# Kernel tuning notes

Measured on AMD Instinct MI355X. Metric: run time of the kernel, lower is better.

Reference implementation:

```python
import jax, jax.numpy as jnp
import numpy as np

N_NODES = 100000
FEAT = 64
HID = 128
N_EDGES = 1200000


def setup_inputs() -> dict:
    key = jax.random.key(0)
    ks = jax.random.split(key, 8)
    x = jax.random.normal(ks[0], (N_NODES, FEAT), dtype=jnp.float32)
    edge_index = jax.random.randint(ks[1], (2, N_EDGES), 0, N_NODES, dtype=jnp.int32)
    # SAGEConv params: lin_l (on aggregated neighbors, with bias), lin_r (on root, no bias)
    W1l = jax.random.normal(ks[2], (HID, FEAT), jnp.float32) / np.float32(np.sqrt(FEAT))
    b1l = jnp.zeros((HID,), jnp.float32)
    W1r = jax.random.normal(ks[3], (HID, FEAT), jnp.float32) / np.float32(np.sqrt(FEAT))
    W2l = jax.random.normal(ks[4], (FEAT, HID), jnp.float32) / np.float32(np.sqrt(HID))
    b2l = jnp.zeros((FEAT,), jnp.float32)
    W2r = jax.random.normal(ks[5], (FEAT, HID), jnp.float32) / np.float32(np.sqrt(HID))
    return {"x": x, "edge_index": edge_index, "W1l": W1l, "b1l": b1l,
            "W1r": W1r, "W2l": W2l, "b2l": b2l, "W2r": W2r}


def _sage_conv(x, src, dst, Wl, bl, Wr, n_nodes):
    # mean aggregation of neighbor messages x[src] at targets dst
    msg = x[src]                                                  # [E, d]
    agg = jax.ops.segment_sum(msg, dst, num_segments=n_nodes)     # [N, d]
    deg = jax.ops.segment_sum(jnp.ones((src.shape[0],), x.dtype), dst,
                              num_segments=n_nodes)               # [N]
    agg = agg / jnp.maximum(deg, 1.0)[:, None]
    # out = lin_l(agg) + lin_r(x); lin_r has no bias (PyG SAGEConv default)
    return agg @ Wl.T + bl + x @ Wr.T


def reference(x, edge_index, W1l, b1l, W1r, W2l, b2l, W2r):
    src, dst = edge_index[0], edge_index[1]
    n = x.shape[0]
    h = jax.nn.relu(_sage_conv(x, src, dst, W1l, b1l, W1r, n))
    # dropout(p=0.5) is identity in eval mode
    out = _sage_conv(h, src, dst, W2l, b2l, W2r, n)
    return out
```

## Files before the change

### kernel.cpp

```cpp
#include <hip/hip_runtime.h>
#include <hip/hip_bf16.h>

typedef __bf16 bf16;
typedef __attribute__((ext_vector_type(8))) __bf16 bf16x8;
typedef __attribute__((ext_vector_type(4))) float f32x4;

#define NBLK 256

__device__ inline void unpack8(uint4 r, f32x4& a, f32x4& b) {
  a.x = __uint_as_float(r.x << 16);
  a.y = __uint_as_float(r.x & 0xffff0000u);
  a.z = __uint_as_float(r.y << 16);
  a.w = __uint_as_float(r.y & 0xffff0000u);
  b.x = __uint_as_float(r.z << 16);
  b.y = __uint_as_float(r.z & 0xffff0000u);
  b.z = __uint_as_float(r.w << 16);
  b.w = __uint_as_float(r.w & 0xffff0000u);
}

__device__ inline uint4 slot_load(const bf16* __restrict__ tab, const int* __restrict__ nbr,
                                  int base, int e, int q, int fo) {
  int idx = base + q;
  uint4 r = make_uint4(0u, 0u, 0u, 0u);
  if (idx < e) {
    int j = nbr[idx];
    r = *(const uint4*)(tab + j * 64 + fo);
  }
  return r;
}

__global__ __launch_bounds__(256) void setup_k(const float* __restrict__ x,
                                               const int* __restrict__ dst,
                                               const float* __restrict__ W1l,
                                               const float* __restrict__ W1r,
                                               const float* __restrict__ W2l,
                                               const float* __restrict__ W2r,
                                               bf16* __restrict__ xb,
                                               bf16* __restrict__ B1,
                                               bf16* __restrict__ B2,
                                               int* __restrict__ hist,
                                               int E, int nb, int N, int Np) {
  __shared__ int h[1024];
  int t = threadIdx.x;
  if (blockIdx.x < NBLK) {
    for (int i = t; i < nb; i += 256) h[i] = 0;
    __syncthreads();
    int chunk = (E + NBLK - 1) / NBLK;
    int s = blockIdx.x * chunk, e = min(E, s + chunk);
    for (int i = s + t; i < e; i += 256) atomicAdd(&h[dst[i] >> 7], 1);
    __syncthreads();
    for (int i = t; i < nb; i += 256) hist[(long)i * NBLK + blockIdx.x] = h[i];
  } else if (blockIdx.x < NBLK + 128) {
    int gid = (blockIdx.x - NBLK) * 256 + t;
    if (gid < 16384) {
      int c = gid >> 7, k = gid & 127;
      float v = (k < 64) ? W1l[c * 64 + k] : W1r[c * 64 + (k - 64)];
      B1[gid] = (bf16)v;
    } else {
      int idx = gid - 16384;
      int n = idx >> 7, k = idx & 127;
      float v = (n < 64) ? W2l[n * 128 + k] : W2r[(n - 64) * 128 + k];
      B2[idx] = (bf16)v;
    }
  } else {
    int gid = (blockIdx.x - NBLK - 128) * 256 + t;
    long base = (long)gid * 4;
    if (base >= (long)Np * 64) return;
    if (base < (long)N * 64) {
      f32x4 v = *(const f32x4*)(x + base);
      bf16 o[4] = {(bf16)v.x, (bf16)v.y, (bf16)v.z, (bf16)v.w};
      *(ulong1*)(xb + base) = *(ulong1*)o;
    } else {
      bf16 o[4] = {(bf16)0.0f, (bf16)0.0f, (bf16)0.0f, (bf16)0.0f};
      *(ulong1*)(xb + base) = *(ulong1*)o;
    }
  }
}

__global__ __launch_bounds__(256) void scanA_k(int* __restrict__ hist,
                                               int* __restrict__ bsum) {
  __shared__ int sd[256];
  int t = threadIdx.x;
  int idx = blockIdx.x * 256 + t;
  int v = hist[idx];
  sd[t] = v;
  __syncthreads();
#pragma unroll
  for (int off = 1; off < 256; off <<= 1) {
    int tv = (t >= off) ? sd[t - off] : 0;
    __syncthreads();
    if (t >= off) sd[t] += tv;
    __syncthreads();
  }
  hist[idx] = sd[t] - v;
  if (t == 255) bsum[blockIdx.x] = sd[255];
}

__global__ __launch_bounds__(1024) void scanB_k(int* __restrict__ bsum, int nb) {
  __shared__ int sd[1024];
  int t = threadIdx.x;
  int v = (t < nb) ? bsum[t] : 0;
  sd[t] = v;
  __syncthreads();
#pragma unroll
  for (int off = 1; off < 1024; off <<= 1) {
    int tv = (t >= off) ? sd[t - off] : 0;
    __syncthreads();
    if (t >= off) sd[t] += tv;
    __syncthreads();
  }
  if (t < nb) bsum[t] = sd[t] - v;
}

__global__ __launch_bounds__(512) void scat_k(const int* __restrict__ src,
                                              const int* __restrict__ dst,
                                              const int* __restrict__ hist,
                                              const int* __restrict__ bsum,
                                              unsigned* __restrict__ ebuf, int E, int nb) {
  __shared__ int cur[1024];
  for (int i = threadIdx.x; i < nb; i += 512)
    cur[i] = bsum[i] + hist[(long)i * NBLK + blockIdx.x];
  __syncthreads();
  int chunk = (E + NBLK - 1) / NBLK;
  int s = blockIdx.x * chunk, e = min(E, s + chunk);
  for (int i = s + threadIdx.x; i < e; i += 512) {
    int d = dst[i];
    int pos = atomicAdd(&cur[d >> 7], 1);
    ebuf[pos] = ((unsigned)src[i] << 7) | (unsigned)(d & 127);
  }
}

__global__ __launch_bounds__(256) void csr_k(const unsigned* __restrict__ ebuf,
                                             const int* __restrict__ bsum,
                                             int* __restrict__ rowptr,
                                             int* __restrict__ nbr, int nb, int Np, int E) {
  __shared__ int hcnt[128];
  __shared__ int hoff[128];
  int b = blockIdx.x, t = threadIdx.x;
  int s = bsum[b];
  int e = (b + 1 < nb) ? bsum[b + 1] : E;
  if (t < 128) hcnt[t] = 0;
  __syncthreads();
  for (int i = s + t; i < e; i += 256) atomicAdd(&hcnt[ebuf[i] & 127u], 1);
  __syncthreads();
  if (t < 128) hoff[t] = hcnt[t];
  __syncthreads();
#pragma unroll
  for (int off = 1; off < 128; off <<= 1) {
    int v = (t < 128 && t >= off) ? hoff[t - off] : 0;
    __syncthreads();
    if (t < 128 && t >= off) hoff[t] += v;
    __syncthreads();
  }
  if (t < 128) {
    int ex = hoff[t] - hcnt[t];
    rowptr[b * 128 + t] = s + ex;
    hcnt[t] = ex;
  }
  if (blockIdx.x == gridDim.x - 1 && t == 0) rowptr[Np] = E;
  __syncthreads();
  for (int i = s + t; i < e; i += 256) {
    unsigned r = ebuf[i];
    int pos = atomicAdd(&hcnt[r & 127u], 1);
    nbr[s + pos] = (int)(r >> 7);
  }
}

__global__ __launch_bounds__(256) void agg1_k(const bf16* __restrict__ xb,
                                              const int* __restrict__ rowptr,
                                              const int* __restrict__ nbr,
                                              bf16* __restrict__ A1, int Np) {
  int wave = threadIdx.x >> 6, lane = threadIdx.x & 63;
  int n = blockIdx.x * 4 + wave;
  if (n >= Np) return;
  int s = rowptr[n], e = rowptr[n + 1];
  int q = lane >> 3, f = lane & 7;
  int fo = f * 8;
  f32x4 sa = {0, 0, 0, 0}, sb = {0, 0, 0, 0};
  uint4 c0 = slot_load(xb, nbr, s, e, q, fo);
  uint4 c1 = slot_load(xb, nbr, s + 8, e, q, fo);
  int i = s + 16;
  for (; i < e; i += 16) {
    uint4 n0 = slot_load(xb, nbr, i, e, q, fo);
    uint4 n1 = slot_load(xb, nbr, i + 8, e, q, fo);
    f32x4 a, b;
    unpack8(c0, a, b); sa += a; sb += b;
    unpack8(c1, a, b); sa += a; sb += b;
    c0 = n0; c1 = n1;
  }
  {
    f32x4 a, b;
    unpack8(c0, a, b); sa += a; sb += b;
    unpack8(c1, a, b); sa += a; sb += b;
  }
  float v[8] = {sa.x, sa.y, sa.z, sa.w, sb.x, sb.y, sb.z, sb.w};
#pragma unroll
  for (int k = 0; k < 8; k++) {
    v[k] += __shfl_xor(v[k], 8);
    v[k] += __shfl_xor(v[k], 16);
    v[k] += __shfl_xor(v[k], 32);
  }
  float invd = 1.0f / fmaxf((float)(e - s), 1.0f);
  if (q == 0) {
    bf16x8 o = {(bf16)(v[0] * invd), (bf16)(v[1] * invd), (bf16)(v[2] * invd),
                (bf16)(v[3] * invd), (bf16)(v[4] * invd), (bf16)(v[5] * invd),
                (bf16)(v[6] * invd), (bf16)(v[7] * invd)};
    *(bf16x8*)(A1 + n * 128 + fo) = o;
  } else if (q == 1) {
    uint4 rv = *(const uint4*)(xb + n * 64 + fo);
    *(uint4*)(A1 + n * 128 + 64 + fo) = rv;
  }
}

__global__ __launch_bounds__(256) void gemm2x_k(const bf16* __restrict__ A,
                                                const bf16* __restrict__ B1,
                                                const bf16* __restrict__ B2,
                                                const float* __restrict__ b1l,
                                                bf16* __restrict__ Ct,
                                                bf16* __restrict__ Cu) {
  __shared__ bf16 hl[4][16][136];
  int wave = threadIdx.x >> 6;
  int lane = threadIdx.x & 63;
  int row = lane & 15;
  int quad = lane >> 4;
  long mbase = (long)blockIdx.x * 64 + (long)wave * 16;

  f32x4 acc[8] = {};
#pragma unroll
  for (int s = 0; s < 4; s++) {
    bf16x8 a0 = *(const bf16x8*)(A + (mbase + row) * 128 + s * 32 + quad * 8);
#pragma unroll
    for (int j = 0; j < 8; j++) {
      bf16x8 bf = *(const bf16x8*)(B1 + (j * 16 + row) * 128 + s * 32 + quad * 8);
      acc[j] = __builtin_amdgcn_mfma_f32_16x16x32_bf16(a0, bf, acc[j], 0, 0, 0);
    }
  }
#pragma unroll
  for (int j = 0; j < 8; j++) {
    int col = j * 16 + row;
    float bv = b1l[col];
#pragma unroll
    for (int i = 0; i < 4; i++) {
      float v = acc[j][i] + bv;
      v = v > 0.0f ? v : 0.0f;
      hl[wave][quad * 4 + i][col] = (bf16)v;
    }
  }

  f32x4 acc2[8] = {};
#pragma unroll
  for (int s = 0; s < 4; s++) {
    bf16x8 a0 = *(const bf16x8*)(&hl[wave][row][s * 32 + quad * 8]);
#pragma unroll
    for (int j = 0; j < 8; j++) {
      bf16x8 bf = *(const bf16x8*)(B2 + (j * 16 + row) * 128 + s * 32 + quad * 8);
      acc2[j] = __builtin_amdgcn_mfma_f32_16x16x32_bf16(a0, bf, acc2[j], 0, 0, 0);
    }
  }
#pragma unroll
  for (int j = 0; j < 8; j++) {
    int col = j * 16 + row;
#pragma unroll
    for (int i = 0; i < 4; i++) {
      float v = acc2[j][i];
      long mrow = mbase + quad * 4 + i;
      if (col < 64) Ct[mrow * 64 + col] = (bf16)v;
      else Cu[mrow * 64 + (col - 64)] = (bf16)v;
    }
  }
}

__global__ __launch_bounds__(256) void agg2_k(const bf16* __restrict__ tmat,
                                              const bf16* __restrict__ umat,
                                              const int* __restrict__ rowptr,
                                              const int* __restrict__ nbr,
                                              const float* __restrict__ b2l,
                                              float* __restrict__ out, int N) {
  int wave = threadIdx.x >> 6, lane = threadIdx.x & 63;
  int n = blockIdx.x * 4 + wave;
  if (n >= N) return;
  int s = rowptr[n], e = rowptr[n + 1];
  int q = lane >> 3, f = lane & 7;
  int fo = f * 8;
  f32x4 sa = {0, 0, 0, 0}, sb = {0, 0, 0, 0};
  uint4 c0 = slot_load(tmat, nbr, s, e, q, fo);
  uint4 c1 = slot_load(tmat, nbr, s + 8, e, q, fo);
  int i = s + 16;
  for (; i < e; i += 16) {
    uint4 n0 = slot_load(tmat, nbr, i, e, q, fo);
    uint4 n1 = slot_load(tmat, nbr, i + 8, e, q, fo);
    f32x4 a, b;
    unpack8(c0, a, b); sa += a; sb += b;
    unpack8(c1, a, b); sa += a; sb += b;
    c0 = n0; c1 = n1;
  }
  {
    f32x4 a, b;
    unpack8(c0, a, b); sa += a; sb += b;
    unpack8(c1, a, b); sa += a; sb += b;
  }
  float v[8] = {sa.x, sa.y, sa.z, sa.w, sb.x, sb.y, sb.z, sb.w};
#pragma unroll
  for (int k = 0; k < 8; k++) {
    v[k] += __shfl_xor(v[k], 8);
    v[k] += __shfl_xor(v[k], 16);
    v[k] += __shfl_xor(v[k], 32);
  }
  if (q == 0) {
    float invd = 1.0f / fmaxf((float)(e - s), 1.0f);
    f32x4 b0 = *(const f32x4*)(b2l + fo);
    f32x4 b1 = *(const f32x4*)(b2l + fo + 4);
    f32x4 ua, ub;
    unpack8(*(const uint4*)(umat + n * 64 + fo), ua, ub);
    f32x4 o0, o1;
    o0.x = v[0] * invd + b0.x + ua.x;
    o0.y = v[1] * invd + b0.y + ua.y;
    o0.z = v[2] * invd + b0.z + ua.z;
    o0.w = v[3] * invd + b0.w + ua.w;
    o1.x = v[4] * invd + b1.x + ub.x;
    o1.y = v[5] * invd + b1.y + ub.y;
    o1.z = v[6] * invd + b1.z + ub.z;
    o1.w = v[7] * invd + b1.w + ub.w;
    *(f32x4*)(out + n * 64 + fo) = o0;
    *(f32x4*)(out + n * 64 + fo + 4) = o1;
  }
}

static inline size_t align256(size_t x) { return (x + 255) / 256 * 256; }

extern "C" void kernel_launch(void* const* d_in, const int* in_sizes, int n_in,
                              void* d_out, int out_size, void* d_ws, size_t ws_size,
                              hipStream_t stream) {
  const float* x = (const float*)d_in[0];
  const int* edge_index = (const int*)d_in[1];
  const float* W1l = (const float*)d_in[2];
  const float* b1l = (const float*)d_in[3];
  const float* W1r = (const float*)d_in[4];
  const float* W2l = (const float*)d_in[5];
  const float* b2l = (const float*)d_in[6];
  const float* W2r = (const float*)d_in[7];

  const int N = in_sizes[0] / 64;
  const int E = in_sizes[1] / 2;
  const int Np = (N + 127) / 128 * 128;
  const int nb = Np / 128;
  const int M = nb * NBLK;

  const int* src = edge_index;
  const int* dst = edge_index + E;

  char* ws = (char*)d_ws;
  size_t off = 0;
  int* hist = (int*)(ws + off);           off += align256((size_t)M * 4);
  int* bsum = (int*)(ws + off);           off += align256((size_t)nb * 4);
  int* rowptr = (int*)(ws + off);         off += align256((size_t)(Np + 1) * 4);
  unsigned* ebuf = (unsigned*)(ws + off); off += align256((size_t)E * 4);
  int* nbr = (int*)(ws + off);            off += align256((size_t)E * 4);
  bf16* xb = (bf16*)(ws + off);           off += align256((size_t)Np * 64 * 2);
  bf16* A1 = (bf16*)(ws + off);           off += align256((size_t)Np * 128 * 2);
  bf16* tmat = (bf16*)(ws + off);         off += align256((size_t)Np * 64 * 2);
  bf16* umat = (bf16*)(ws + off);         off += align256((size_t)Np * 64 * 2);
  bf16* B1 = (bf16*)(ws + off);           off += align256(128 * 128 * 2);
  bf16* B2 = (bf16*)(ws + off);           off += align256(128 * 128 * 2);
  float* out = (float*)d_out;

  const int cvtBlocks = (int)(((long)Np * 64 / 4 + 255) / 256);
  setup_k<<<NBLK + 128 + cvtBlocks, 256, 0, stream>>>(x, dst, W1l, W1r, W2l, W2r,
                                                      xb, B1, B2, hist, E, nb, N, Np);
  scanA_k<<<nb, 256, 0, stream>>>(hist, bsum);
  scanB_k<<<1, 1024, 0, stream>>>(bsum, nb);
  scat_k<<<NBLK, 512, 0, stream>>>(src, dst, hist, bsum, ebuf, E, nb);
  csr_k<<<nb, 256, 0, stream>>>(ebuf, bsum, rowptr, nbr, nb, Np, E);

  agg1_k<<<Np / 4, 256, 0, stream>>>(xb, rowptr, nbr, A1, Np);
  gemm2x_k<<<Np / 64, 256, 0, stream>>>(A1, B1, B2, b1l, tmat, umat);
  agg2_k<<<(N + 3) / 4, 256, 0, stream>>>(tmat, umat, rowptr, nbr, b2l, out, N);
}
```

Measured before the change: 257.7 us.

## Make dual GEMM persistent with register-resident weights and double-buffered A tiles

```diff
diff --git a/kernel.cpp b/kernel.cpp
--- a/kernel.cpp
+++ b/kernel.cpp
@@ -212,61 +212,103 @@
   }
 }
 
-__global__ __launch_bounds__(256) void gemm2x_k(const bf16* __restrict__ A,
-                                                const bf16* __restrict__ B1,
-                                                const bf16* __restrict__ B2,
-                                                const float* __restrict__ b1l,
-                                                bf16* __restrict__ Ct,
-                                                bf16* __restrict__ Cu) {
-  __shared__ bf16 hl[4][16][136];
-  int wave = threadIdx.x >> 6;
-  int lane = threadIdx.x & 63;
-  int row = lane & 15;
-  int quad = lane >> 4;
-  long mbase = (long)blockIdx.x * 64 + (long)wave * 16;
-
-  f32x4 acc[8] = {};
-#pragma unroll
-  for (int s = 0; s < 4; s++) {
-    bf16x8 a0 = *(const bf16x8*)(A + (mbase + row) * 128 + s * 32 + quad * 8);
-#pragma unroll
-    for (int j = 0; j < 8; j++) {
-      bf16x8 bf = *(const bf16x8*)(B1 + (j * 16 + row) * 128 + s * 32 + quad * 8);
-      acc[j] = __builtin_amdgcn_mfma_f32_16x16x32_bf16(a0, bf, acc[j], 0, 0, 0);
-    }
-  }
-#pragma unroll
-  for (int j = 0; j < 8; j++) {
-    int col = j * 16 + row;
-    float bv = b1l[col];
-#pragma unroll
-    for (int i = 0; i < 4; i++) {
-      float v = acc[j][i] + bv;
-      v = v > 0.0f ? v : 0.0f;
-      hl[wave][quad * 4 + i][col] = (bf16)v;
-    }
-  }
-
-  f32x4 acc2[8] = {};
-#pragma unroll
-  for (int s = 0; s < 4; s++) {
-    bf16x8 a0 = *(const bf16x8*)(&hl[wave][row][s * 32 + quad * 8]);
-#pragma unroll
-    for (int j = 0; j < 8; j++) {
-      bf16x8 bf = *(const bf16x8*)(B2 + (j * 16 + row) * 128 + s * 32 + quad * 8);
-      acc2[j] = __builtin_amdgcn_mfma_f32_16x16x32_bf16(a0, bf, acc2[j], 0, 0, 0);
-    }
-  }
-#pragma unroll
-  for (int j = 0; j < 8; j++) {
-    int col = j * 16 + row;
-#pragma unroll
-    for (int i = 0; i < 4; i++) {
-      float v = acc2[j][i];
-      long mrow = mbase + quad * 4 + i;
-      if (col < 64) Ct[mrow * 64 + col] = (bf16)v;
-      else Cu[mrow * 64 + (col - 64)] = (bf16)v;
-    }
+__device__ inline int swzoff(int r, int x) {
+  return r * 256 + (x ^ (((r & 3) << 6) ^ ((r & 7) << 4)));
+}
+
+__global__ __launch_bounds__(256) void fused_k(const bf16* __restrict__ A,
+                                               const bf16* __restrict__ B1g,
+                                               const bf16* __restrict__ B2g,
+                                               const float* __restrict__ b1l,
+                                               bf16* __restrict__ Ct,
+                                               bf16* __restrict__ Cu, int T) {
+  __shared__ __align__(16) char Asm[2][8192];
+  __shared__ __align__(16) char Hsm[8192];
+  int tid = threadIdx.x;
+  int wave = tid >> 6, lane = tid & 63;
+  int row = lane & 15, quad = lane >> 4;
+  int cb = wave * 32;
+
+  bf16x8 b1f[2][4], b2f[2][4];
+#pragma unroll
+  for (int jj = 0; jj < 2; jj++)
+#pragma unroll
+    for (int s = 0; s < 4; s++) {
+      b1f[jj][s] = *(const bf16x8*)(B1g + (cb + jj * 16 + row) * 128 + s * 32 + quad * 8);
+      b2f[jj][s] = *(const bf16x8*)(B2g + (cb + jj * 16 + row) * 128 + s * 32 + quad * 8);
+    }
+  float bias[2] = {b1l[cb + row], b1l[cb + 16 + row]};
+
+  int srow = wave * 8 + quad;
+  int schunk = row;
+
+  int t = blockIdx.x;
+  {
+    uint4 v0 = *(const uint4*)(A + ((long)t * 32 + srow) * 128 + schunk * 8);
+    uint4 v1 = *(const uint4*)(A + ((long)t * 32 + srow + 4) * 128 + schunk * 8);
+    *(uint4*)(Asm[0] + swzoff(srow, schunk * 16)) = v0;
+    *(uint4*)(Asm[0] + swzoff(srow + 4, schunk * 16)) = v1;
+  }
+  __syncthreads();
+
+  int p = 0;
+  for (; t < T; t += (int)gridDim.x, p ^= 1) {
+    int tn = t + (int)gridDim.x;
+    bool pf = tn < T;
+    uint4 v0 = {}, v1 = {};
+    if (pf) {
+      v0 = *(const uint4*)(A + ((long)tn * 32 + srow) * 128 + schunk * 8);
+      v1 = *(const uint4*)(A + ((long)tn * 32 + srow + 4) * 128 + schunk * 8);
+    }
+    f32x4 acc1[2][2] = {};
+#pragma unroll
+    for (int s = 0; s < 4; s++) {
+#pragma unroll
+      for (int st = 0; st < 2; st++) {
+        bf16x8 a = *(const bf16x8*)(Asm[p] + swzoff(st * 16 + row, s * 64 + quad * 16));
+#pragma unroll
+        for (int jj = 0; jj < 2; jj++)
+          acc1[st][jj] = __builtin_amdgcn_mfma_f32_16x16x32_bf16(a, b1f[jj][s], acc1[st][jj], 0, 0, 0);
+      }
+    }
+#pragma unroll
+    for (int st = 0; st < 2; st++)
+#pragma unroll
+      for (int jj = 0; jj < 2; jj++)
+#pragma unroll
+        for (int i = 0; i < 4; i++) {
+          float v = acc1[st][jj][i] + bias[jj];
+          v = v > 0.0f ? v : 0.0f;
+          *(bf16*)(Hsm + swzoff(st * 16 + quad * 4 + i, (cb + jj * 16 + row) * 2)) = (bf16)v;
+        }
+    __syncthreads();
+    f32x4 acc2[2][2] = {};
+#pragma unroll
+    for (int s = 0; s < 4; s++) {
+#pragma unroll
+      for (int st = 0; st < 2; st++) {
+        bf16x8 a = *(const bf16x8*)(Hsm + swzoff(st * 16 + row, s * 64 + quad * 16));
+#pragma unroll
+        for (int jj = 0; jj < 2; jj++)
+          acc2[st][jj] = __builtin_amdgcn_mfma_f32_16x16x32_bf16(a, b2f[jj][s], acc2[st][jj], 0, 0, 0);
+      }
+    }
+    bf16* outp = (wave < 2) ? Ct : Cu;
+    int oc = cb + row - ((wave < 2) ? 0 : 64);
+#pragma unroll
+    for (int st = 0; st < 2; st++)
+#pragma unroll
+      for (int jj = 0; jj < 2; jj++)
+#pragma unroll
+        for (int i = 0; i < 4; i++) {
+          long grow = (long)t * 32 + st * 16 + quad * 4 + i;
+          outp[grow * 64 + oc + jj * 16] = (bf16)acc2[st][jj][i];
+        }
+    if (pf) {
+      *(uint4*)(Asm[p ^ 1] + swzoff(srow, schunk * 16)) = v0;
+      *(uint4*)(Asm[p ^ 1] + swzoff(srow + 4, schunk * 16)) = v1;
+    }
+    __syncthreads();
   }
 }
 
@@ -373,6 +415,6 @@
   csr_k<<<nb, 256, 0, stream>>>(ebuf, bsum, rowptr, nbr, nb, Np, E);
 
   agg1_k<<<Np / 4, 256, 0, stream>>>(xb, rowptr, nbr, A1, Np);
-  gemm2x_k<<<Np / 64, 256, 0, stream>>>(A1, B1, B2, b1l, tmat, umat);
+  fused_k<<<1024, 256, 0, stream>>>(A1, B1, B2, b1l, tmat, umat, Np / 32);
   agg2_k<<<(N + 3) / 4, 256, 0, stream>>>(tmat, umat, rowptr, nbr, b2l, out, N);
 }
```

Result: faster. 219.2 us (-14.9%).
